# Optimization experiments

Measured on AMD Instinct MI355X. Metric: run time of the kernel, lower is better.

Reference implementation:

```python
import jax, jax.numpy as jnp
import numpy as np

V, G, F, T = 500000, 25000, 256, 2


def setup_inputs() -> dict:
    key = jax.random.key(0)
    ks = jax.random.split(key, 10)
    s = 1.0 / np.sqrt(F)
    node_feats = jax.random.normal(ks[0], (V, F), jnp.float32)
    seg_ids = jnp.sort(jax.random.randint(ks[1], (V,), 0, G, dtype=jnp.int32))
    Wl = jax.random.uniform(ks[2], (T, 1, 2 * F), jnp.float32, -s, s)
    bl = jax.random.uniform(ks[3], (T, 1), jnp.float32, -s, s)
    Wp = jax.random.uniform(ks[4], (T, F, F), jnp.float32, -s, s)
    bp = jax.random.uniform(ks[5], (T, F), jnp.float32, -s, s)
    Wih = jax.random.uniform(ks[6], (T, 3 * F, F), jnp.float32, -s, s)
    Whh = jax.random.uniform(ks[7], (T, 3 * F, F), jnp.float32, -s, s)
    bih = jax.random.uniform(ks[8], (T, 3 * F), jnp.float32, -s, s)
    bhh = jax.random.uniform(ks[9], (T, 3 * F), jnp.float32, -s, s)
    return dict(node_feats=node_feats, seg_ids=seg_ids, Wl=Wl, bl=bl,
                Wp=Wp, bp=bp, Wih=Wih, Whh=Whh, bih=bih, bhh=bhh)


def _segment_softmax(z, seg):
    # z: (V,) per-node logits; softmax within each graph segment
    m = jax.ops.segment_max(z, seg, num_segments=G)
    m = jnp.where(jnp.isfinite(m), m, 0.0)  # guard empty segments
    e = jnp.exp(z - m[seg])
    d = jax.ops.segment_sum(e, seg, num_segments=G)
    return e / d[seg]


def _gru_cell(x, h, Wih, Whh, bih, bhh):
    # torch.nn.GRUCell semantics
    gi = x @ Wih.T + bih  # (G, 3F)
    gh = h @ Whh.T + bhh
    ir, iz, inn = jnp.split(gi, 3, axis=1)
    hr, hz, hn = jnp.split(gh, 3, axis=1)
    r = jax.nn.sigmoid(ir + hr)
    zg = jax.nn.sigmoid(iz + hz)
    n = jnp.tanh(inn + r * hn)
    return (1.0 - zg) * n + zg * h


def reference(node_feats, seg_ids, Wl, bl, Wp, bp, Wih, Whh, bih, bhh):
    # initial graph feats = sum of node feats per graph
    g_feats = jax.ops.segment_sum(node_feats, seg_ids, num_segments=G)  # (G, F)
    for t in range(T):
        ctx_in = jnp.concatenate([jax.nn.relu(g_feats)[seg_ids], node_feats], axis=1)  # (V, 2F)
        z = jax.nn.leaky_relu(ctx_in @ Wl[t].T + bl[t], 0.01)[:, 0]  # (V,)
        a = _segment_softmax(z, seg_ids)[:, None]  # (V, 1)
        hv = node_feats @ Wp[t].T + bp[t]  # dropout=0 -> identity
        g_repr = jax.ops.segment_sum(a * hv, seg_ids, num_segments=G)  # (G, F)
        context = jax.nn.elu(g_repr)
        g_feats = _gru_cell(context, g_feats, Wih[t], Whh[t], bih[t], bhh[t])
    return g_feats
```

## Files before the change

### kernel.cpp

```cpp
#include <hip/hip_runtime.h>
#include <cstdint>

typedef unsigned short u16;
typedef unsigned int u32;

#define V_N 500000
#define G_N 25000
#define F_N 256
#define GP_N 25088

typedef __attribute__((ext_vector_type(8))) __bf16 bf16x8;
typedef __attribute__((ext_vector_type(4))) float f32x4;

__device__ __forceinline__ u16 f2bf(float f) {
  u32 u = __builtin_bit_cast(u32, f);
  u += 0x7fffu + ((u >> 16) & 1u);
  return (u16)(u >> 16);
}
__device__ __forceinline__ float bf2f(u16 s) {
  u32 u = ((u32)s) << 16;
  return __builtin_bit_cast(float, u);
}
__device__ __forceinline__ float sigm(float x) { return 1.f / (1.f + __expf(-x)); }
__device__ __forceinline__ float tanh_fast(float x) {
  return 1.f - 2.f / (__expf(2.f * x) + 1.f);
}
__device__ __forceinline__ float lrelu(float z) { return z >= 0.f ? z : 0.01f * z; }

template <int CTRL>
__device__ __forceinline__ float dpp_add_f(float v) {
  int t = __builtin_amdgcn_update_dpp(0, __builtin_bit_cast(int, v), CTRL, 0xF, 0xF, true);
  return v + __builtin_bit_cast(float, t);
}
template <int CTRL>
__device__ __forceinline__ float dpp_max_f(float v) {
  int t = __builtin_amdgcn_update_dpp(0, __builtin_bit_cast(int, v), CTRL, 0xF, 0xF, true);
  return fmaxf(v, __builtin_bit_cast(float, t));
}
__device__ __forceinline__ float wave_sum(float v) {
  v = dpp_add_f<0xB1>(v);
  v = dpp_add_f<0x4E>(v);
  v = dpp_add_f<0x141>(v);
  v = dpp_add_f<0x140>(v);
  v += __shfl_xor(v, 16, 64);
  v += __shfl_xor(v, 32, 64);
  return v;
}
__device__ __forceinline__ float wave_max(float v) {
  v = dpp_max_f<0xB1>(v);
  v = dpp_max_f<0x4E>(v);
  v = dpp_max_f<0x141>(v);
  v = dpp_max_f<0x140>(v);
  v = fmaxf(v, __shfl_xor(v, 16, 64));
  v = fmaxf(v, __shfl_xor(v, 32, 64));
  return v;
}

__device__ __forceinline__ void load_lds16(const void* g, void* l) {
  __builtin_amdgcn_global_load_lds(
      (const __attribute__((address_space(1))) void*)g,
      (__attribute__((address_space(3))) void*)l, 16, 0, 0);
}

#define CONVW_BLK 4608
#define OFFS_BLK ((V_N + 1 + 255) / 256)
__global__ __launch_bounds__(256) void k_prep(const float* __restrict__ Wp,
                                              const float* __restrict__ Wih,
                                              const float* __restrict__ Whh,
                                              u16* __restrict__ Wpb, u16* __restrict__ W3,
                                              const int* __restrict__ seg, int* __restrict__ off) {
  if (blockIdx.x >= CONVW_BLK) {
    int v = (blockIdx.x - CONVW_BLK) * 256 + threadIdx.x;
    if (v > V_N) return;
    if (v == 0) {
      int c = seg[0];
      for (int g = 0; g <= c; ++g) off[g] = 0;
    } else if (v == V_N) {
      int pr = seg[V_N - 1];
      for (int g = pr + 1; g <= G_N; ++g) off[g] = V_N;
    } else {
      int pr = seg[v - 1], c = seg[v];
      for (int g = pr + 1; g <= c; ++g) off[g] = v;
    }
    return;
  }
  int i = blockIdx.x * 256 + threadIdx.x;
  const int NP = 2 * F_N * F_N;
  if (i < NP) {
    Wpb[i] = f2bf(Wp[i]);
    return;
  }
  int j = i - NP;
  int t = j >> 19;
  int r = j & 524287;
  int row = r >> 9;
  int k = r & 511;
  int q = row >> 6;
  int gate = (row >> 4) & 3;
  int c = q * 16 + (row & 15);
  const float* wi = Wih + t * 196608;
  const float* wh = Whh + t * 196608;
  float v;
  if (gate == 0) {
    v = (k < 256) ? wi[c * 256 + k] : wh[c * 256 + (k - 256)];
  } else if (gate == 1) {
    v = (k < 256) ? wi[(256 + c) * 256 + k] : wh[(256 + c) * 256 + (k - 256)];
  } else if (gate == 2) {
    v = (k < 256) ? wi[(512 + c) * 256 + k] : 0.f;
  } else {
    v = (k >= 256) ? wh[(512 + c) * 256 + (k - 256)] : 0.f;
  }
  W3[j] = f2bf(v);
}

__global__ __launch_bounds__(256) void k_node_fused(const float* __restrict__ nf,
                                                    const int* __restrict__ off,
                                                    const float* __restrict__ Wl,
                                                    const float* __restrict__ bl,
                                                    u16* __restrict__ xb,
                                                    float* __restrict__ q0, float* __restrict__ q1,
                                                    float* __restrict__ hbuf0, u16* __restrict__ x2a,
                                                    u16* __restrict__ x2b,
                                                    u16* __restrict__ sb, float* __restrict__ Ag) {
  int g = blockIdx.x * 4 + (threadIdx.x >> 6);
  int lane = threadIdx.x & 63;
  if (g >= GP_N) return;
  if (g >= G_N) {
    float4 z4 = {0.f, 0.f, 0.f, 0.f};
    uint2 z2 = {0u, 0u};
    *reinterpret_cast<float4*>(hbuf0 + (size_t)g * F_N + lane * 4) = z4;
    *reinterpret_cast<uint2*>(x2a + (size_t)g * 512 + 256 + lane * 4) = z2;
    *reinterpret_cast<uint2*>(x2b + (size_t)g * 512 + 256 + lane * 4) = z2;
    *reinterpret_cast<uint2*>(sb + (size_t)g * F_N + lane * 4) = z2;
    if (lane == 0) Ag[g] = 0.f;
    return;
  }
  const float4 w0 = *reinterpret_cast<const float4*>(Wl + 256 + lane * 4);
  const float4 w1 = *reinterpret_cast<const float4*>(Wl + 768 + lane * 4);
  const float4 wh = *reinterpret_cast<const float4*>(Wl + lane * 4);
  int s = off[g], e = off[g + 1];
  int n = e - s;
  float a0 = 0.f, a1 = 0.f, a2 = 0.f, a3 = 0.f;
  float qreg = 0.f;
  int v = s;
  for (; v + 2 <= e; v += 2) {
    const float4 xA = *reinterpret_cast<const float4*>(nf + (size_t)v * F_N + lane * 4);
    const float4 xB = *reinterpret_cast<const float4*>(nf + (size_t)(v + 1) * F_N + lane * 4);
    a0 += xA.x + xB.x; a1 += xA.y + xB.y; a2 += xA.z + xB.z; a3 += xA.w + xB.w;
    uint2 pA, pB;
    pA.x = (u32)f2bf(xA.x) | ((u32)f2bf(xA.y) << 16);
    pA.y = (u32)f2bf(xA.z) | ((u32)f2bf(xA.w) << 16);
    pB.x = (u32)f2bf(xB.x) | ((u32)f2bf(xB.y) << 16);
    pB.y = (u32)f2bf(xB.z) | ((u32)f2bf(xB.w) << 16);
    *reinterpret_cast<uint2*>(xb + (size_t)v * F_N + lane * 4) = pA;
    *reinterpret_cast<uint2*>(xb + (size_t)(v + 1) * F_N + lane * 4) = pB;
    float dA0 = wave_sum(xA.x * w0.x + xA.y * w0.y + xA.z * w0.z + xA.w * w0.w);
    float dA1 = wave_sum(xA.x * w1.x + xA.y * w1.y + xA.z * w1.z + xA.w * w1.w);
    float dB0 = wave_sum(xB.x * w0.x + xB.y * w0.y + xB.z * w0.z + xB.w * w0.w);
    float dB1 = wave_sum(xB.x * w1.x + xB.y * w1.y + xB.z * w1.z + xB.w * w1.w);
    if (lane == 0) {
      q0[v] = dA0; q1[v] = dA1;
      q0[v + 1] = dB0; q1[v + 1] = dB1;
    }
    int li = v - s;
    if (li == lane) qreg = dA0;
    if (li + 1 == lane) qreg = dB0;
  }
  if (v < e) {
    const float4 xA = *reinterpret_cast<const float4*>(nf + (size_t)v * F_N + lane * 4);
    a0 += xA.x; a1 += xA.y; a2 += xA.z; a3 += xA.w;
    uint2 pA;
    pA.x = (u32)f2bf(xA.x) | ((u32)f2bf(xA.y) << 16);
    pA.y = (u32)f2bf(xA.z) | ((u32)f2bf(xA.w) << 16);
    *reinterpret_cast<uint2*>(xb + (size_t)v * F_N + lane * 4) = pA;
    float dA0 = wave_sum(xA.x * w0.x + xA.y * w0.y + xA.z * w0.z + xA.w * w0.w);
    float dA1 = wave_sum(xA.x * w1.x + xA.y * w1.y + xA.z * w1.z + xA.w * w1.w);
    if (lane == 0) { q0[v] = dA0; q1[v] = dA1; }
    if (v - s == lane) qreg = dA0;
  }
  float4 h4 = {a0, a1, a2, a3};
  *reinterpret_cast<float4*>(hbuf0 + (size_t)g * F_N + lane * 4) = h4;
  uint2 hs;
  hs.x = (u32)f2bf(a0) | ((u32)f2bf(a1) << 16);
  hs.y = (u32)f2bf(a2) | ((u32)f2bf(a3) << 16);
  *reinterpret_cast<uint2*>(x2a + (size_t)g * 512 + 256 + lane * 4) = hs;

  if (n == 0) {
    if (lane < 32) {
      uint4 z = {0u, 0u, 0u, 0u};
      *reinterpret_cast<uint4*>(sb + (size_t)g * F_N + lane * 8) = z;
    }
    if (lane == 0) Ag[g] = 0.f;
    return;
  }
  float p = wave_sum(fmaxf(a0, 0.f) * wh.x + fmaxf(a1, 0.f) * wh.y +
                     fmaxf(a2, 0.f) * wh.z + fmaxf(a3, 0.f) * wh.w) + bl[0];

  float mx, inv, ee = 0.f;
  bool fast = (n <= 64);
  if (fast) {
    float z = (lane < n) ? lrelu(p + qreg) : -3.4e38f;
    mx = wave_max(z);
    ee = (lane < n) ? __expf(z - mx) : 0.f;
    inv = 1.f / wave_sum(ee);
    asm volatile("s_waitcnt vmcnt(0)" ::: "memory");
  } else {
    asm volatile("s_waitcnt vmcnt(0)" ::: "memory");
    float mloc = -3.4e38f;
    for (int i = lane; i < n; i += 64) mloc = fmaxf(mloc, lrelu(p + q0[s + i]));
    mx = wave_max(mloc);
    float dloc = 0.f;
    for (int i = lane; i < n; i += 64) dloc += __expf(lrelu(p + q0[s + i]) - mx);
    inv = 1.f / wave_sum(dloc);
  }

  int half = lane >> 5;
  int cl = (lane & 31) * 8;
  float acc[8] = {0.f, 0.f, 0.f, 0.f, 0.f, 0.f, 0.f, 0.f};
  for (int i = 0; i < n; i += 2) {
    int r = i + half;
    float a;
    if (fast) {
      float ev = __shfl(ee, (r < 64 ? r : 63), 64);
      a = (r < n) ? ev * inv : 0.f;
    } else {
      a = (r < n) ? __expf(lrelu(p + q0[s + r]) - mx) * inv : 0.f;
    }
    int row = s + (r < n ? r : 0);
    uint4 x = *reinterpret_cast<const uint4*>(xb + (size_t)row * F_N + cl);
    acc[0] += a * bf2f((u16)(x.x & 0xffff));
    acc[1] += a * bf2f((u16)(x.x >> 16));
    acc[2] += a * bf2f((u16)(x.y & 0xffff));
    acc[3] += a * bf2f((u16)(x.y >> 16));
    acc[4] += a * bf2f((u16)(x.z & 0xffff));
    acc[5] += a * bf2f((u16)(x.z >> 16));
    acc[6] += a * bf2f((u16)(x.w & 0xffff));
    acc[7] += a * bf2f((u16)(x.w >> 16));
  }
#pragma unroll
  for (int k = 0; k < 8; ++k) acc[k] += __shfl_xor(acc[k], 32, 64);
  if (lane < 32) {
    uint4 o;
    o.x = (u32)f2bf(acc[0]) | ((u32)f2bf(acc[1]) << 16);
    o.y = (u32)f2bf(acc[2]) | ((u32)f2bf(acc[3]) << 16);
    o.z = (u32)f2bf(acc[4]) | ((u32)f2bf(acc[5]) << 16);
    o.w = (u32)f2bf(acc[6]) | ((u32)f2bf(acc[7]) << 16);
    *reinterpret_cast<uint4*>(sb + (size_t)g * F_N + cl) = o;
  }
  if (lane == 0) Ag[g] = 1.f;
}

__global__ __launch_bounds__(256) void k_attn(const float* __restrict__ h,
                                              const u16* __restrict__ xb,
                                              const float* __restrict__ q,
                                              const int* __restrict__ off,
                                              const float* __restrict__ Wl,
                                              const float* __restrict__ bl, int t,
                                              u16* __restrict__ sb, float* __restrict__ Ag) {
  int g = blockIdx.x * 4 + (threadIdx.x >> 6);
  int lane = threadIdx.x & 63;
  if (g >= G_N) return;

  const float4 hv = *reinterpret_cast<const float4*>(h + (size_t)g * F_N + lane * 4);
  const float4 wv = *reinterpret_cast<const float4*>(Wl + t * 512 + lane * 4);
  float p = wave_sum(fmaxf(hv.x, 0.f) * wv.x + fmaxf(hv.y, 0.f) * wv.y +
                     fmaxf(hv.z, 0.f) * wv.z + fmaxf(hv.w, 0.f) * wv.w) + bl[t];

  int s = off[g], n = off[g + 1] - s;
  if (n == 0) {
    if (lane < 32) {
      uint4 z = {0u, 0u, 0u, 0u};
      *reinterpret_cast<uint4*>(sb + (size_t)g * F_N + lane * 8) = z;
    }
    if (lane == 0) Ag[g] = 0.f;
    return;
  }
  float mloc = -3.4e38f;
  for (int i = lane; i < n; i += 64) mloc = fmaxf(mloc, lrelu(p + q[s + i]));
  float mx = wave_max(mloc);
  float dloc = 0.f;
  for (int i = lane; i < n; i += 64) dloc += __expf(lrelu(p + q[s + i]) - mx);
  float inv = 1.f / wave_sum(dloc);

  int half = lane >> 5;
  int cl = (lane & 31) * 8;
  float acc[8] = {0.f, 0.f, 0.f, 0.f, 0.f, 0.f, 0.f, 0.f};
  for (int i = 0; i < n; i += 2) {
    int r = i + half;
    float a = 0.f;
    int row = s;
    if (r < n) {
      a = __expf(lrelu(p + q[s + r]) - mx) * inv;
      row = s + r;
    }
    uint4 x = *reinterpret_cast<const uint4*>(xb + (size_t)row * F_N + cl);
    acc[0] += a * bf2f((u16)(x.x & 0xffff));
    acc[1] += a * bf2f((u16)(x.x >> 16));
    acc[2] += a * bf2f((u16)(x.y & 0xffff));
    acc[3] += a * bf2f((u16)(x.y >> 16));
    acc[4] += a * bf2f((u16)(x.z & 0xffff));
    acc[5] += a * bf2f((u16)(x.z >> 16));
    acc[6] += a * bf2f((u16)(x.w & 0xffff));
    acc[7] += a * bf2f((u16)(x.w >> 16));
  }
#pragma unroll
  for (int k = 0; k < 8; ++k) acc[k] += __shfl_xor(acc[k], 32, 64);
  if (lane < 32) {
    uint4 o;
    o.x = (u32)f2bf(acc[0]) | ((u32)f2bf(acc[1]) << 16);
    o.y = (u32)f2bf(acc[2]) | ((u32)f2bf(acc[3]) << 16);
    o.z = (u32)f2bf(acc[4]) | ((u32)f2bf(acc[5]) << 16);
    o.w = (u32)f2bf(acc[6]) | ((u32)f2bf(acc[7]) << 16);
    *reinterpret_cast<uint4*>(sb + (size_t)g * F_N + cl) = o;
  }
  if (lane == 0) Ag[g] = 1.f;
}

__global__ __launch_bounds__(256) void k_gemm(const u16* __restrict__ A, const u16* __restrict__ B,
                                              int K, float* __restrict__ dst,
                                              u16* __restrict__ x2out, const float* __restrict__ AgH,
                                              const float* __restrict__ b1, const float* __restrict__ b2,
                                              int mode, int writehb) {
  __shared__ __align__(16) u16 As[128 * 64];
  __shared__ __align__(16) u16 Bs[128 * 64];
  int tid = threadIdx.x, lane = tid & 63, w = tid >> 6;
  int gy = gridDim.y;
  int l = blockIdx.y * gridDim.x + blockIdx.x;
  int chunk = (gridDim.x * gy) >> 3;
  int tau = (l & 7) * chunk + (l >> 3);
  int m0 = (tau / gy) * 128, n0 = (tau % gy) * 128;
  int nby = tau % gy;
  int wm = w >> 1, wn = w & 1;
  f32x4 zero = {0.f, 0.f, 0.f, 0.f};
  f32x4 acc[4][4];
#pragma unroll
  for (int i = 0; i < 4; ++i)
#pragma unroll
    for (int j = 0; j < 4; ++j) acc[i][j] = zero;

  int rowA = tid >> 3;
  int col8 = (tid & 7) * 8;
  for (int k0 = 0; k0 < K; k0 += 64) {
    __syncthreads();
#pragma unroll
    for (int c = 0; c < 4; ++c) {
      int r = c * 32 + rowA;
      const u16* gA = A + (size_t)(m0 + r) * K + k0 + col8;
      const u16* gB = B + (size_t)(n0 + r) * K + k0 + col8;
      char* lA = (char*)As + (c * 256 + w * 64) * 16;
      char* lB = (char*)Bs + (c * 256 + w * 64) * 16;
      load_lds16(gA, lA);
      load_lds16(gB, lB);
    }
    __syncthreads();
#pragma unroll
    for (int kk = 0; kk < 64; kk += 32) {
      bf16x8 af[4], bfr[4];
#pragma unroll
      for (int i = 0; i < 4; ++i) {
        af[i] = *reinterpret_cast<const bf16x8*>(&As[(wm * 64 + i * 16 + (lane & 15)) * 64 + kk + (lane >> 4) * 8]);
        bfr[i] = *reinterpret_cast<const bf16x8*>(&Bs[(wn * 64 + i * 16 + (lane & 15)) * 64 + kk + (lane >> 4) * 8]);
      }
#pragma unroll
      for (int i = 0; i < 4; ++i)
#pragma unroll
        for (int j = 0; j < 4; ++j)
          acc[i][j] = __builtin_amdgcn_mfma_f32_16x16x32_bf16(af[i], bfr[j], acc[i][j], 0, 0, 0);
    }
  }
  int crow0 = m0 + wm * 64 + (lane >> 4) * 4;
  if (mode == 1) {
    int ccol0 = n0 + wn * 64 + (lane & 15);
#pragma unroll
    for (int i = 0; i < 4; ++i)
#pragma unroll
      for (int j = 0; j < 4; ++j) {
        int col = ccol0 + j * 16;
#pragma unroll
        for (int r = 0; r < 4; ++r) {
          int row = crow0 + i * 16 + r;
          float v = acc[i][j][r] + AgH[row] * b1[col];
          v = v > 0.f ? v : (__expf(v) - 1.f);
          x2out[(size_t)row * 512 + col] = f2bf(v);
        }
      }
  } else {
    int qgrp = nby * 2 + wn;
    int c = qgrp * 16 + (lane & 15);
    float bi0 = b1[c] + b2[c];
    float bi1 = b1[256 + c] + b2[256 + c];
    float bi2 = b1[512 + c];
    float bi3 = b2[512 + c];
#pragma unroll
    for (int i = 0; i < 4; ++i)
#pragma unroll
      for (int r = 0; r < 4; ++r) {
        int grow = crow0 + i * 16 + r;
        if (grow >= G_N) continue;
        float ir = acc[i][0][r] + bi0;
        float iz = acc[i][1][r] + bi1;
        float nn = acc[i][2][r] + bi2;
        float hn = acc[i][3][r] + bi3;
        float rg = sigm(ir);
        float zg = sigm(iz);
        float h0 = AgH[(size_t)grow * F_N + c];
        float nv = tanh_fast(nn + rg * hn);
        float hN = (1.f - zg) * nv + zg * h0;
        dst[(size_t)grow * F_N + c] = hN;
        if (writehb) x2out[(size_t)grow * 512 + 256 + c] = f2bf(hN);
      }
  }
}

extern "C" void kernel_launch(void* const* d_in, const int* in_sizes, int n_in,
                              void* d_out, int out_size, void* d_ws, size_t ws_size,
                              hipStream_t stream) {
  const float* nf = (const float*)d_in[0];
  const int* seg = (const int*)d_in[1];
  const float* Wl = (const float*)d_in[2];
  const float* bl = (const float*)d_in[3];
  const float* Wp = (const float*)d_in[4];
  const float* bp = (const float*)d_in[5];
  const float* Wih = (const float*)d_in[6];
  const float* Whh = (const float*)d_in[7];
  const float* bih = (const float*)d_in[8];
  const float* bhh = (const float*)d_in[9];
  float* out = (float*)d_out;

  char* p = (char*)d_ws;
  auto alloc = [&](size_t bytes) {
    char* r = p;
    p += (bytes + 511) & ~(size_t)511;
    return r;
  };
  float* q0 = (float*)alloc((size_t)V_N * 4);
  float* q1 = (float*)alloc((size_t)V_N * 4);
  int* off = (int*)alloc((size_t)(G_N + 1) * 4);
  float* hbuf0 = (float*)alloc((size_t)GP_N * F_N * 4);
  float* hbuf1 = (float*)alloc((size_t)GP_N * F_N * 4);
  u16* sb = (u16*)alloc((size_t)GP_N * F_N * 2);
  float* Ag = (float*)alloc((size_t)GP_N * 4);
  u16* X2a = (u16*)alloc((size_t)GP_N * 512 * 2);
  u16* X2b = (u16*)alloc((size_t)GP_N * 512 * 2);
  u16* Wpb = (u16*)alloc((size_t)2 * F_N * F_N * 2);
  u16* W3 = (u16*)alloc((size_t)2 * 1024 * 512 * 2);
  u16* xb = (u16*)alloc((size_t)V_N * F_N * 2);

  k_prep<<<CONVW_BLK + OFFS_BLK, 256, 0, stream>>>(Wp, Wih, Whh, Wpb, W3, seg, off);
  k_node_fused<<<GP_N / 4, 256, 0, stream>>>(nf, off, Wl, bl, xb, q0, q1,
                                             hbuf0, X2a, X2b, sb, Ag);

  k_gemm<<<dim3(196, 2), 256, 0, stream>>>(sb, Wpb, 256,
                                           nullptr, X2a, Ag, bp, nullptr, 1, 0);
  k_gemm<<<dim3(196, 8), 256, 0, stream>>>(X2a, W3, 512,
                                           hbuf1, X2b, hbuf0, bih, bhh, 2, 1);
  k_attn<<<G_N / 4, 256, 0, stream>>>(hbuf1, xb, q1, off, Wl, bl, 1, sb, Ag);
  k_gemm<<<dim3(196, 2), 256, 0, stream>>>(sb, Wpb + 65536, 256,
                                           nullptr, X2b, Ag, bp + 256, nullptr, 1, 0);
  k_gemm<<<dim3(196, 8), 256, 0, stream>>>(X2b, W3 + 524288, 512,
                                           out, nullptr, hbuf1, bih + 768, bhh + 768, 2, 0);
}
```

Baseline: 464.6 us.

## Fuse prep into node kernel, binary-search offsets, skip zero GRU MFMA blocks

Folds the weight conversion and segment-offset kernel into the node kernel: each wave binary-searches the sorted segment ids for its own start and end instead of reading a precomputed offsets array, and extra blocks convert the weights. This removes one launch and the serialization between prep and node processing. The GRU GEMM now skips MFMAs for the all-zero quarter of the packed W3 layout (the input-new gate over the h half and the hidden-new gate over the x half). The costs are a binary search per wave and a data-dependent branch inside the unrolled MFMA loop.

Result: no change. 468.0 us (+0.7%).

```diff
diff --git a/kernel.cpp b/kernel.cpp
--- a/kernel.cpp
+++ b/kernel.cpp
@@ -8,6 +8,9 @@
 #define G_N 25000
 #define F_N 256
 #define GP_N 25088
+
+#define NODE_BLK (GP_N / 4)
+#define CONVW_BLK 4608
 
 typedef __attribute__((ext_vector_type(8))) __bf16 bf16x8;
 typedef __attribute__((ext_vector_type(4))) float f32x4;
@@ -62,70 +65,56 @@
       (__attribute__((address_space(3))) void*)l, 16, 0, 0);
 }
 
-#define CONVW_BLK 4608
-#define OFFS_BLK ((V_N + 1 + 255) / 256)
-__global__ __launch_bounds__(256) void k_prep(const float* __restrict__ Wp,
-                                              const float* __restrict__ Wih,
-                                              const float* __restrict__ Whh,
-                                              u16* __restrict__ Wpb, u16* __restrict__ W3,
-                                              const int* __restrict__ seg, int* __restrict__ off) {
-  if (blockIdx.x >= CONVW_BLK) {
-    int v = (blockIdx.x - CONVW_BLK) * 256 + threadIdx.x;
-    if (v > V_N) return;
-    if (v == 0) {
-      int c = seg[0];
-      for (int g = 0; g <= c; ++g) off[g] = 0;
-    } else if (v == V_N) {
-      int pr = seg[V_N - 1];
-      for (int g = pr + 1; g <= G_N; ++g) off[g] = V_N;
-    } else {
-      int pr = seg[v - 1], c = seg[v];
-      for (int g = pr + 1; g <= c; ++g) off[g] = v;
-    }
-    return;
-  }
-  int i = blockIdx.x * 256 + threadIdx.x;
-  const int NP = 2 * F_N * F_N;
-  if (i < NP) {
-    Wpb[i] = f2bf(Wp[i]);
-    return;
-  }
-  int j = i - NP;
-  int t = j >> 19;
-  int r = j & 524287;
-  int row = r >> 9;
-  int k = r & 511;
-  int q = row >> 6;
-  int gate = (row >> 4) & 3;
-  int c = q * 16 + (row & 15);
-  const float* wi = Wih + t * 196608;
-  const float* wh = Whh + t * 196608;
-  float v;
-  if (gate == 0) {
-    v = (k < 256) ? wi[c * 256 + k] : wh[c * 256 + (k - 256)];
-  } else if (gate == 1) {
-    v = (k < 256) ? wi[(256 + c) * 256 + k] : wh[(256 + c) * 256 + (k - 256)];
-  } else if (gate == 2) {
-    v = (k < 256) ? wi[(512 + c) * 256 + k] : 0.f;
-  } else {
-    v = (k >= 256) ? wh[(512 + c) * 256 + (k - 256)] : 0.f;
-  }
-  W3[j] = f2bf(v);
-}
-
 __global__ __launch_bounds__(256) void k_node_fused(const float* __restrict__ nf,
-                                                    const int* __restrict__ off,
+                                                    const int* __restrict__ seg,
                                                     const float* __restrict__ Wl,
                                                     const float* __restrict__ bl,
                                                     u16* __restrict__ xb,
                                                     float* __restrict__ q0, float* __restrict__ q1,
                                                     float* __restrict__ hbuf0, u16* __restrict__ x2a,
                                                     u16* __restrict__ x2b,
-                                                    u16* __restrict__ sb, float* __restrict__ Ag) {
+                                                    u16* __restrict__ sb, float* __restrict__ Ag,
+                                                    int* __restrict__ off,
+                                                    const float* __restrict__ Wp,
+                                                    const float* __restrict__ Wih,
+                                                    const float* __restrict__ Whh,
+                                                    u16* __restrict__ Wpb, u16* __restrict__ W3) {
+  if (blockIdx.x >= NODE_BLK) {
+    int i = (blockIdx.x - NODE_BLK) * 256 + threadIdx.x;
+    const int NP = 2 * F_N * F_N;
+    if (i < NP) {
+      Wpb[i] = f2bf(Wp[i]);
+      return;
+    }
+    int j = i - NP;
+    int t = j >> 19;
+    int r = j & 524287;
+    int row = r >> 9;
+    int k = r & 511;
+    int q = row >> 6;
+    int gate = (row >> 4) & 3;
+    int c = q * 16 + (row & 15);
+    const float* wi = Wih + t * 196608;
+    const float* wh = Whh + t * 196608;
+    float v;
+    if (gate == 0) {
+      v = (k < 256) ? wi[c * 256 + k] : wh[c * 256 + (k - 256)];
+    } else if (gate == 1) {
+      v = (k < 256) ? wi[(256 + c) * 256 + k] : wh[(256 + c) * 256 + (k - 256)];
+    } else if (gate == 2) {
+      v = (k < 256) ? wi[(512 + c) * 256 + k] : 0.f;
+    } else {
+      v = (k >= 256) ? wh[(512 + c) * 256 + (k - 256)] : 0.f;
+    }
+    W3[j] = f2bf(v);
+    return;
+  }
+
   int g = blockIdx.x * 4 + (threadIdx.x >> 6);
   int lane = threadIdx.x & 63;
-  if (g >= GP_N) return;
   if (g >= G_N) {
+    if (g == G_N && lane == 0) off[G_N] = V_N;
+    if (g >= GP_N) return;
     float4 z4 = {0.f, 0.f, 0.f, 0.f};
     uint2 z2 = {0u, 0u};
     *reinterpret_cast<float4*>(hbuf0 + (size_t)g * F_N + lane * 4) = z4;
@@ -135,119 +124,132 @@
     if (lane == 0) Ag[g] = 0.f;
     return;
   }
-  const float4 w0 = *reinterpret_cast<const float4*>(Wl + 256 + lane * 4);
-  const float4 w1 = *reinterpret_cast<const float4*>(Wl + 768 + lane * 4);
-  const float4 wh = *reinterpret_cast<const float4*>(Wl + lane * 4);
-  int s = off[g], e = off[g + 1];
-  int n = e - s;
-  float a0 = 0.f, a1 = 0.f, a2 = 0.f, a3 = 0.f;
-  float qreg = 0.f;
-  int v = s;
-  for (; v + 2 <= e; v += 2) {
-    const float4 xA = *reinterpret_cast<const float4*>(nf + (size_t)v * F_N + lane * 4);
-    const float4 xB = *reinterpret_cast<const float4*>(nf + (size_t)(v + 1) * F_N + lane * 4);
-    a0 += xA.x + xB.x; a1 += xA.y + xB.y; a2 += xA.z + xB.z; a3 += xA.w + xB.w;
-    uint2 pA, pB;
-    pA.x = (u32)f2bf(xA.x) | ((u32)f2bf(xA.y) << 16);
-    pA.y = (u32)f2bf(xA.z) | ((u32)f2bf(xA.w) << 16);
-    pB.x = (u32)f2bf(xB.x) | ((u32)f2bf(xB.y) << 16);
-    pB.y = (u32)f2bf(xB.z) | ((u32)f2bf(xB.w) << 16);
-    *reinterpret_cast<uint2*>(xb + (size_t)v * F_N + lane * 4) = pA;
-    *reinterpret_cast<uint2*>(xb + (size_t)(v + 1) * F_N + lane * 4) = pB;
-    float dA0 = wave_sum(xA.x * w0.x + xA.y * w0.y + xA.z * w0.z + xA.w * w0.w);
-    float dA1 = wave_sum(xA.x * w1.x + xA.y * w1.y + xA.z * w1.z + xA.w * w1.w);
-    float dB0 = wave_sum(xB.x * w0.x + xB.y * w0.y + xB.z * w0.z + xB.w * w0.w);
-    float dB1 = wave_sum(xB.x * w1.x + xB.y * w1.y + xB.z * w1.z + xB.w * w1.w);
-    if (lane == 0) {
-      q0[v] = dA0; q1[v] = dA1;
-      q0[v + 1] = dB0; q1[v + 1] = dB1;
-    }
-    int li = v - s;
-    if (li == lane) qreg = dA0;
-    if (li + 1 == lane) qreg = dB0;
-  }
-  if (v < e) {
-    const float4 xA = *reinterpret_cast<const float4*>(nf + (size_t)v * F_N + lane * 4);
-    a0 += xA.x; a1 += xA.y; a2 += xA.z; a3 += xA.w;
-    uint2 pA;
-    pA.x = (u32)f2bf(xA.x) | ((u32)f2bf(xA.y) << 16);
-    pA.y = (u32)f2bf(xA.z) | ((u32)f2bf(xA.w) << 16);
-    *reinterpret_cast<uint2*>(xb + (size_t)v * F_N + lane * 4) = pA;
-    float dA0 = wave_sum(xA.x * w0.x + xA.y * w0.y + xA.z * w0.z + xA.w * w0.w);
-    float dA1 = wave_sum(xA.x * w1.x + xA.y * w1.y + xA.z * w1.z + xA.w * w1.w);
-    if (lane == 0) { q0[v] = dA0; q1[v] = dA1; }
-    if (v - s == lane) qreg = dA0;
-  }
-  float4 h4 = {a0, a1, a2, a3};
-  *reinterpret_cast<float4*>(hbuf0 + (size_t)g * F_N + lane * 4) = h4;
-  uint2 hs;
-  hs.x = (u32)f2bf(a0) | ((u32)f2bf(a1) << 16);
-  hs.y = (u32)f2bf(a2) | ((u32)f2bf(a3) << 16);
-  *reinterpret_cast<uint2*>(x2a + (size_t)g * 512 + 256 + lane * 4) = hs;
-
-  if (n == 0) {
+  {
+    int tgt = g + (lane & 1);
+    int lo = 0, hi = V_N;
+    while (lo < hi) {
+      int mid = (lo + hi) >> 1;
+      bool lt = seg[mid] < tgt;
+      lo = lt ? mid + 1 : lo;
+      hi = lt ? hi : mid;
+    }
+    int s_ = __shfl(lo, 0, 64);
+    int e_ = __shfl(lo, 1, 64);
+    if (lane == 0) off[g] = s_;
+    const float4 w0 = *reinterpret_cast<const float4*>(Wl + 256 + lane * 4);
+    const float4 w1 = *reinterpret_cast<const float4*>(Wl + 768 + lane * 4);
+    const float4 wh = *reinterpret_cast<const float4*>(Wl + lane * 4);
+    int s = s_, e = e_;
+    int n = e - s;
+    float a0 = 0.f, a1 = 0.f, a2 = 0.f, a3 = 0.f;
+    float qreg = 0.f;
+    int v = s;
+    for (; v + 2 <= e; v += 2) {
+      const float4 xA = *reinterpret_cast<const float4*>(nf + (size_t)v * F_N + lane * 4);
+      const float4 xB = *reinterpret_cast<const float4*>(nf + (size_t)(v + 1) * F_N + lane * 4);
+      a0 += xA.x + xB.x; a1 += xA.y + xB.y; a2 += xA.z + xB.z; a3 += xA.w + xB.w;
+      uint2 pA, pB;
+      pA.x = (u32)f2bf(xA.x) | ((u32)f2bf(xA.y) << 16);
+      pA.y = (u32)f2bf(xA.z) | ((u32)f2bf(xA.w) << 16);
+      pB.x = (u32)f2bf(xB.x) | ((u32)f2bf(xB.y) << 16);
+      pB.y = (u32)f2bf(xB.z) | ((u32)f2bf(xB.w) << 16);
+      *reinterpret_cast<uint2*>(xb + (size_t)v * F_N + lane * 4) = pA;
+      *reinterpret_cast<uint2*>(xb + (size_t)(v + 1) * F_N + lane * 4) = pB;
+      float dA0 = wave_sum(xA.x * w0.x + xA.y * w0.y + xA.z * w0.z + xA.w * w0.w);
+      float dA1 = wave_sum(xA.x * w1.x + xA.y * w1.y + xA.z * w1.z + xA.w * w1.w);
+      float dB0 = wave_sum(xB.x * w0.x + xB.y * w0.y + xB.z * w0.z + xB.w * w0.w);
+      float dB1 = wave_sum(xB.x * w1.x + xB.y * w1.y + xB.z * w1.z + xB.w * w1.w);
+      if (lane == 0) {
+        q0[v] = dA0; q1[v] = dA1;
+        q0[v + 1] = dB0; q1[v + 1] = dB1;
+      }
+      int li = v - s;
+      if (li == lane) qreg = dA0;
+      if (li + 1 == lane) qreg = dB0;
+    }
+    if (v < e) {
+      const float4 xA = *reinterpret_cast<const float4*>(nf + (size_t)v * F_N + lane * 4);
+      a0 += xA.x; a1 += xA.y; a2 += xA.z; a3 += xA.w;
+      uint2 pA;
+      pA.x = (u32)f2bf(xA.x) | ((u32)f2bf(xA.y) << 16);
+      pA.y = (u32)f2bf(xA.z) | ((u32)f2bf(xA.w) << 16);
+      *reinterpret_cast<uint2*>(xb + (size_t)v * F_N + lane * 4) = pA;
+      float dA0 = wave_sum(xA.x * w0.x + xA.y * w0.y + xA.z * w0.z + xA.w * w0.w);
+      float dA1 = wave_sum(xA.x * w1.x + xA.y * w1.y + xA.z * w1.z + xA.w * w1.w);
+      if (lane == 0) { q0[v] = dA0; q1[v] = dA1; }
+      if (v - s == lane) qreg = dA0;
+    }
+    float4 h4 = {a0, a1, a2, a3};
+    *reinterpret_cast<float4*>(hbuf0 + (size_t)g * F_N + lane * 4) = h4;
+    uint2 hs;
+    hs.x = (u32)f2bf(a0) | ((u32)f2bf(a1) << 16);
+    hs.y = (u32)f2bf(a2) | ((u32)f2bf(a3) << 16);
+    *reinterpret_cast<uint2*>(x2a + (size_t)g * 512 + 256 + lane * 4) = hs;
+
+    if (n == 0) {
+      if (lane < 32) {
+        uint4 z = {0u, 0u, 0u, 0u};
+        *reinterpret_cast<uint4*>(sb + (size_t)g * F_N + lane * 8) = z;
+      }
+      if (lane == 0) Ag[g] = 0.f;
+      return;
+    }
+    float p = wave_sum(fmaxf(a0, 0.f) * wh.x + fmaxf(a1, 0.f) * wh.y +
+                       fmaxf(a2, 0.f) * wh.z + fmaxf(a3, 0.f) * wh.w) + bl[0];
+
+    float mx, inv, ee = 0.f;
+    bool fast = (n <= 64);
+    if (fast) {
+      float z = (lane < n) ? lrelu(p + qreg) : -3.4e38f;
+      mx = wave_max(z);
+      ee = (lane < n) ? __expf(z - mx) : 0.f;
+      inv = 1.f / wave_sum(ee);
+      asm volatile("s_waitcnt vmcnt(0)" ::: "memory");
+    } else {
+      asm volatile("s_waitcnt vmcnt(0)" ::: "memory");
+      float mloc = -3.4e38f;
+      for (int i = lane; i < n; i += 64) mloc = fmaxf(mloc, lrelu(p + q0[s + i]));
+      mx = wave_max(mloc);
+      float dloc = 0.f;
+      for (int i = lane; i < n; i += 64) dloc += __expf(lrelu(p + q0[s + i]) - mx);
+      inv = 1.f / wave_sum(dloc);
+    }
+
+    int half = lane >> 5;
+    int cl = (lane & 31) * 8;
+    float acc[8] = {0.f, 0.f, 0.f, 0.f, 0.f, 0.f, 0.f, 0.f};
+    for (int i = 0; i < n; i += 2) {
+      int r = i + half;
+      float a;
+      if (fast) {
+        float ev = __shfl(ee, (r < 64 ? r : 63), 64);
+        a = (r < n) ? ev * inv : 0.f;
+      } else {
+        a = (r < n) ? __expf(lrelu(p + q0[s + r]) - mx) * inv : 0.f;
+      }
+      int row = s + (r < n ? r : 0);
+      uint4 x = *reinterpret_cast<const uint4*>(xb + (size_t)row * F_N + cl);
+      acc[0] += a * bf2f((u16)(x.x & 0xffff));
+      acc[1] += a * bf2f((u16)(x.x >> 16));
+      acc[2] += a * bf2f((u16)(x.y & 0xffff));
+      acc[3] += a * bf2f((u16)(x.y >> 16));
+      acc[4] += a * bf2f((u16)(x.z & 0xffff));
+      acc[5] += a * bf2f((u16)(x.z >> 16));
+      acc[6] += a * bf2f((u16)(x.w & 0xffff));
+      acc[7] += a * bf2f((u16)(x.w >> 16));
+    }
+#pragma unroll
+    for (int k = 0; k < 8; ++k) acc[k] += __shfl_xor(acc[k], 32, 64);
     if (lane < 32) {
-      uint4 z = {0u, 0u, 0u, 0u};
-      *reinterpret_cast<uint4*>(sb + (size_t)g * F_N + lane * 8) = z;
-    }
-    if (lane == 0) Ag[g] = 0.f;
-    return;
-  }
-  float p = wave_sum(fmaxf(a0, 0.f) * wh.x + fmaxf(a1, 0.f) * wh.y +
-                     fmaxf(a2, 0.f) * wh.z + fmaxf(a3, 0.f) * wh.w) + bl[0];
-
-  float mx, inv, ee = 0.f;
-  bool fast = (n <= 64);
-  if (fast) {
-    float z = (lane < n) ? lrelu(p + qreg) : -3.4e38f;
-    mx = wave_max(z);
-    ee = (lane < n) ? __expf(z - mx) : 0.f;
-    inv = 1.f / wave_sum(ee);
-    asm volatile("s_waitcnt vmcnt(0)" ::: "memory");
-  } else {
-    asm volatile("s_waitcnt vmcnt(0)" ::: "memory");
-    float mloc = -3.4e38f;
-    for (int i = lane; i < n; i += 64) mloc = fmaxf(mloc, lrelu(p + q0[s + i]));
-    mx = wave_max(mloc);
-    float dloc = 0.f;
-    for (int i = lane; i < n; i += 64) dloc += __expf(lrelu(p + q0[s + i]) - mx);
-    inv = 1.f / wave_sum(dloc);
-  }
-
-  int half = lane >> 5;
-  int cl = (lane & 31) * 8;
-  float acc[8] = {0.f, 0.f, 0.f, 0.f, 0.f, 0.f, 0.f, 0.f};
-  for (int i = 0; i < n; i += 2) {
-    int r = i + half;
-    float a;
-    if (fast) {
-      float ev = __shfl(ee, (r < 64 ? r : 63), 64);
-      a = (r < n) ? ev * inv : 0.f;
-    } else {
-      a = (r < n) ? __expf(lrelu(p + q0[s + r]) - mx) * inv : 0.f;
-    }
-    int row = s + (r < n ? r : 0);
-    uint4 x = *reinterpret_cast<const uint4*>(xb + (size_t)row * F_N + cl);
-    acc[0] += a * bf2f((u16)(x.x & 0xffff));
-    acc[1] += a * bf2f((u16)(x.x >> 16));
-    acc[2] += a * bf2f((u16)(x.y & 0xffff));
-    acc[3] += a * bf2f((u16)(x.y >> 16));
-    acc[4] += a * bf2f((u16)(x.z & 0xffff));
-    acc[5] += a * bf2f((u16)(x.z >> 16));
-    acc[6] += a * bf2f((u16)(x.w & 0xffff));
-    acc[7] += a * bf2f((u16)(x.w >> 16));
-  }
-#pragma unroll
-  for (int k = 0; k < 8; ++k) acc[k] += __shfl_xor(acc[k], 32, 64);
-  if (lane < 32) {
-    uint4 o;
-    o.x = (u32)f2bf(acc[0]) | ((u32)f2bf(acc[1]) << 16);
-    o.y = (u32)f2bf(acc[2]) | ((u32)f2bf(acc[3]) << 16);
-    o.z = (u32)f2bf(acc[4]) | ((u32)f2bf(acc[5]) << 16);
-    o.w = (u32)f2bf(acc[6]) | ((u32)f2bf(acc[7]) << 16);
-    *reinterpret_cast<uint4*>(sb + (size_t)g * F_N + cl) = o;
-  }
-  if (lane == 0) Ag[g] = 1.f;
+      uint4 o;
+      o.x = (u32)f2bf(acc[0]) | ((u32)f2bf(acc[1]) << 16);
+      o.y = (u32)f2bf(acc[2]) | ((u32)f2bf(acc[3]) << 16);
+      o.z = (u32)f2bf(acc[4]) | ((u32)f2bf(acc[5]) << 16);
+      o.w = (u32)f2bf(acc[6]) | ((u32)f2bf(acc[7]) << 16);
+      *reinterpret_cast<uint4*>(sb + (size_t)g * F_N + cl) = o;
+    }
+    if (lane == 0) Ag[g] = 1.f;
+  }
 }
 
 __global__ __launch_bounds__(256) void k_attn(const float* __restrict__ h,
@@ -353,19 +355,21 @@
       load_lds16(gB, lB);
     }
     __syncthreads();
+    int jskip = (mode == 2) ? ((k0 < 256) ? 3 : 2) : -1;
 #pragma unroll
     for (int kk = 0; kk < 64; kk += 32) {
-      bf16x8 af[4], bfr[4];
-#pragma unroll
-      for (int i = 0; i < 4; ++i) {
+      bf16x8 af[4];
+#pragma unroll
+      for (int i = 0; i < 4; ++i)
         af[i] = *reinterpret_cast<const bf16x8*>(&As[(wm * 64 + i * 16 + (lane & 15)) * 64 + kk + (lane >> 4) * 8]);
-        bfr[i] = *reinterpret_cast<const bf16x8*>(&Bs[(wn * 64 + i * 16 + (lane & 15)) * 64 + kk + (lane >> 4) * 8]);
-      }
-#pragma unroll
-      for (int i = 0; i < 4; ++i)
-#pragma unroll
-        for (int j = 0; j < 4; ++j)
-          acc[i][j] = __builtin_amdgcn_mfma_f32_16x16x32_bf16(af[i], bfr[j], acc[i][j], 0, 0, 0);
+#pragma unroll
+      for (int j = 0; j < 4; ++j) {
+        if (j == jskip) continue;
+        bf16x8 bfr = *reinterpret_cast<const bf16x8*>(&Bs[(wn * 64 + j * 16 + (lane & 15)) * 64 + kk + (lane >> 4) * 8]);
+#pragma unroll
+        for (int i = 0; i < 4; ++i)
+          acc[i][j] = __builtin_amdgcn_mfma_f32_16x16x32_bf16(af[i], bfr, acc[i][j], 0, 0, 0);
+      }
     }
   }
   int crow0 = m0 + wm * 64 + (lane >> 4) * 4;
@@ -446,9 +450,9 @@
   u16* W3 = (u16*)alloc((size_t)2 * 1024 * 512 * 2);
   u16* xb = (u16*)alloc((size_t)V_N * F_N * 2);
 
-  k_prep<<<CONVW_BLK + OFFS_BLK, 256, 0, stream>>>(Wp, Wih, Whh, Wpb, W3, seg, off);
-  k_node_fused<<<GP_N / 4, 256, 0, stream>>>(nf, off, Wl, bl, xb, q0, q1,
-                                             hbuf0, X2a, X2b, sb, Ag);
+  k_node_fused<<<NODE_BLK + CONVW_BLK, 256, 0, stream>>>(
+      nf, seg, Wl, bl, xb, q0, q1, hbuf0, X2a, X2b, sb, Ag, off,
+      Wp, Wih, Whh, Wpb, W3);
 
   k_gemm<<<dim3(196, 2), 256, 0, stream>>>(sb, Wpb, 256,
                                            nullptr, X2a, Ag, bp, nullptr, 1, 0);
```
